# Optimization experiments

Hardware: AMD Instinct MI355X
Metric: run time of the kernel (lower is better)

The kernel has to match this reference:

```python
import jax, jax.numpy as jnp
import numpy as np

N = 10000      # nodes
E = 320000     # edges
F_IN = 33      # input node features
H = 32         # hidden
G = 64         # graphs in batch


def setup_inputs() -> dict:
    key = jax.random.key(0)
    ks = jax.random.split(key, 24)
    s = 0.1  # small init scale for numerical sanity
    inp = {
        "x": jax.random.normal(ks[0], (N, F_IN), jnp.float32),
        "edge_index": jax.random.randint(ks[1], (2, E), 0, N, jnp.int32),
        "edge_attr": jax.random.uniform(ks[2], (E, 1), jnp.float32),
        "batch": jnp.sort(jax.random.randint(ks[3], (N,), 0, G, jnp.int32)),
        # conv1: edge-MLP Linear(1 -> F_IN*H), root weight [F_IN,H], bias [H]
        "nn_w1": jax.random.normal(ks[4], (1, F_IN * H), jnp.float32) * s,
        "nn_b1": jax.random.normal(ks[5], (F_IN * H,), jnp.float32) * s,
        "root1": jax.random.normal(ks[6], (F_IN, H), jnp.float32) * s,
        "bias1": jnp.zeros((H,), jnp.float32),
        # conv2: edge-MLP Linear(1 -> H*H)
        "nn_w2": jax.random.normal(ks[7], (1, H * H), jnp.float32) * s,
        "nn_b2": jax.random.normal(ks[8], (H * H,), jnp.float32) * s,
        "root2": jax.random.normal(ks[9], (H, H), jnp.float32) * s,
        "bias2": jnp.zeros((H,), jnp.float32),
        # conv3
        "nn_w3": jax.random.normal(ks[10], (1, H * H), jnp.float32) * s,
        "nn_b3": jax.random.normal(ks[11], (H * H,), jnp.float32) * s,
        "root3": jax.random.normal(ks[12], (H, H), jnp.float32) * s,
        "bias3": jnp.zeros((H,), jnp.float32),
        # readout MLP: Linear(3H -> H), Linear(H -> 2)
        "lin1_w": jax.random.normal(ks[13], (3 * H, H), jnp.float32) * s,
        "lin1_b": jnp.zeros((H,), jnp.float32),
        "lin2_w": jax.random.normal(ks[14], (H, 2), jnp.float32) * s,
        "lin2_b": jnp.zeros((2,), jnp.float32),
    }
    return inp


def _nnconv(x, src, dst, edge_attr, nn_w, nn_b, root, bias):
    """PyG NNConv (aggr='add'): out_i = x_i @ root + bias + sum_{e: dst(e)=i} x_{src(e)} @ Theta(e_attr)."""
    in_dim, out_dim = root.shape
    # per-edge weight matrix from edge MLP: [E, in, out]
    W = (edge_attr @ nn_w + nn_b).reshape(-1, in_dim, out_dim)
    msg = jnp.einsum('ei,eio->eo', x[src], W)          # gather + per-edge small matmul
    agg = jax.ops.segment_sum(msg, dst, num_segments=N)  # scatter-add into targets
    return agg + x @ root + bias


def reference(x, edge_index, edge_attr, batch,
              nn_w1, nn_b1, root1, bias1,
              nn_w2, nn_b2, root2, bias2,
              nn_w3, nn_b3, root3, bias3,
              lin1_w, lin1_b, lin2_w, lin2_b):
    src, dst = edge_index[0], edge_index[1]
    h = jax.nn.relu(_nnconv(x, src, dst, edge_attr, nn_w1, nn_b1, root1, bias1))
    h = jax.nn.relu(_nnconv(h, src, dst, edge_attr, nn_w2, nn_b2, root2, bias2))
    h = jax.nn.relu(_nnconv(h, src, dst, edge_attr, nn_w3, nn_b3, root3, bias3))
    # global add / mean / max pooling over graphs
    add_p = jax.ops.segment_sum(h, batch, num_segments=G)
    cnt = jax.ops.segment_sum(jnp.ones((N, 1), h.dtype), batch, num_segments=G)
    mean_p = add_p / jnp.maximum(cnt, 1.0)
    max_p = jax.ops.segment_max(h, batch, num_segments=G)
    max_p = jnp.where(jnp.isfinite(max_p), max_p, 0.0)  # guard empty segments
    g = jnp.concatenate([add_p, mean_p, max_p], axis=1)  # [G, 3H]
    g = jax.nn.relu(g @ lin1_w + lin1_b)
    # dropout p=0.5 is identity in eval mode
    logits = g @ lin2_w + lin2_b
    return jax.nn.log_softmax(logits, axis=-1)
```

## Files before the change

### kernel.cpp

```cpp
#include <hip/hip_runtime.h>

constexpr int N_  = 10000;
constexpr int E_  = 320000;
constexpr int F1  = 33;
constexpr int H   = 32;
constexpr int G   = 64;
constexpr int CAP = 96;
constexpr int NB_ = 1280;
constexpr int ROW = CAP * 8;

constexpr int EBLK = E_ / 256;
constexpr int PBLK = N_ / 8;
constexpr int SLICES = 32;
constexpr int CHUNKS = 16;
constexpr int TILE   = 640;
constexpr int AT    = 1024;
constexpr int ITERS = TILE / 128;

__device__ __forceinline__ unsigned bf16r(float x) {
    unsigned u = __float_as_uint(x);
    return (u + 0x7FFFu + ((u >> 16) & 1u)) >> 16;
}

__device__ __forceinline__ size_t mslot(int n, int pos) {
    return (size_t)(n >> 3) * ROW + (size_t)(pos >> 3) * 64 + (n & 7) * 8 + (pos & 7);
}


__global__ __launch_bounds__(256) void k_build_pre1(
        const int* __restrict__ ei, const float* __restrict__ ea,
        const float* __restrict__ x, const int* __restrict__ batch,
        const float* __restrict__ A, const float* __restrict__ Bm,
        const float* __restrict__ Rw, const float* __restrict__ bias,
        int* __restrict__ counts, unsigned* __restrict__ meta2,
        unsigned* __restrict__ UVs, float* __restrict__ Rs,
        int* __restrict__ startsP) {
    __shared__ unsigned s_uv[32][9];
    __shared__ float    s_r[32][9];
    if (blockIdx.x < EBLK) {
        int e = blockIdx.x * 256 + threadIdx.x;
        int s = ei[e];
        int d = ei[E_ + e];
        int pos = atomicAdd(&counts[d], 1);
        meta2[mslot(d, pos)] = (unsigned)s | (bf16r(ea[e]) << 16);
    } else {
        int base8 = (blockIdx.x - EBLK) * 8;
        int grp = threadIdx.x >> 5;
        int f = threadIdx.x & 31;
        int node = base8 + grp;
        if (f == 0) {
            int b = batch[node];
            int bp = (node == 0) ? -1 : batch[node - 1];
            if (b != bp) startsP[b] = node + 1;
        }
        float u = 0.f, v = 0.f, r = bias[f];
        const float* xr = x + (size_t)node * F1;
        #pragma unroll
        for (int k = 0; k < F1; ++k) {
            float xv = xr[k];
            u = fmaf(xv, A[k * H + f], u);
            v = fmaf(xv, Bm[k * H + f], v);
            r = fmaf(xv, Rw[k * H + f], r);
        }
        s_uv[f][grp] = bf16r(u) | (bf16r(v) << 16);
        s_r[f][grp]  = r;
        __syncthreads();
        int fo = threadIdx.x >> 3;
        int nl = threadIdx.x & 7;
        UVs[(size_t)fo * N_ + base8 + nl] = s_uv[fo][nl];
        Rs [(size_t)fo * N_ + base8 + nl] = s_r [fo][nl];
    }
}


__global__ __launch_bounds__(256) void k_pre(
        const float* __restrict__ Hs,
        const float* __restrict__ A, const float* __restrict__ Bm,
        const float* __restrict__ Rw, const float* __restrict__ bias,
        unsigned* __restrict__ UVs, float* __restrict__ Rs) {
    __shared__ unsigned s_uv[32][9];
    __shared__ float    s_r[32][9];
    int base8 = blockIdx.x * 8;
    int grp = threadIdx.x >> 5;
    int f = threadIdx.x & 31;
    int node = base8 + grp;
    float hv = Hs[(size_t)f * N_ + node];
    float u = 0.f, v = 0.f, r = bias[f];
    #pragma unroll
    for (int k = 0; k < H; ++k) {
        float hk = __shfl(hv, k, 32);
        u = fmaf(hk, A[k * H + f], u);
        v = fmaf(hk, Bm[k * H + f], v);
        r = fmaf(hk, Rw[k * H + f], r);
    }
    s_uv[f][grp] = bf16r(u) | (bf16r(v) << 16);
    s_r[f][grp]  = r;
    __syncthreads();
    int fo = threadIdx.x >> 3;
    int nl = threadIdx.x & 7;
    UVs[(size_t)fo * N_ + base8 + nl] = s_uv[fo][nl];
    Rs [(size_t)fo * N_ + base8 + nl] = s_r [fo][nl];
}


__global__ __launch_bounds__(1024, 8) void k_agg_lds(
        const int* __restrict__ counts, const unsigned* __restrict__ meta2,
        const unsigned* __restrict__ UVs, const float* __restrict__ Rs,
        float* __restrict__ Hs) {
    __shared__ __align__(16) unsigned uvl[N_];
    int s     = blockIdx.x & 31;
    int chunk = blockIdx.x >> 5;

    int l   = threadIdx.x & 63;
    int wav = threadIdx.x >> 6;
    int j0  = l & 7;
    int nl  = l >> 3;

    int cbase = chunk * TILE + wav * 8;
    int node = cbase + nl;
    int nc = min(node, N_ - 1);
    int dg = (node < N_) ? counts[nc] : 0;
    float rv = Rs[(size_t)s * N_ + nc];
    const unsigned* mrow = meta2 + (size_t)(cbase >> 3) * ROW + l;
    unsigned m0 = mrow[0], m1 = mrow[64], m2 = mrow[128],
             m3 = mrow[192], m4 = mrow[256], m5 = mrow[320];

    const unsigned* srcp = UVs + (size_t)s * N_;
    #pragma unroll
    for (int i = 0; i < 3; ++i) {
        int d4 = (i * AT + (int)threadIdx.x) * 4;
        if (d4 + 4 <= N_) {
            uint4 t = *reinterpret_cast<const uint4*>(srcp + d4);
            *reinterpret_cast<uint4*>(&uvl[d4]) = t;
        }
    }
    __syncthreads();

    for (int it = 0; it < ITERS; ++it) {
        int nbase = cbase + 128;
        int nnode = nbase + nl;
        int nnc = min(nnode, N_ - 1);
        int ndg = 0; float nrv = 0.f;
        unsigned n0 = 0, n1 = 0, n2 = 0, n3 = 0, n4 = 0, n5 = 0;
        if (it < ITERS - 1) {
            ndg = (nnode < N_) ? counts[nnc] : 0;
            nrv = Rs[(size_t)s * N_ + nnc];
            const unsigned* nmr = meta2 + (size_t)(nbase >> 3) * ROW + l;
            n0 = nmr[0]; n1 = nmr[64]; n2 = nmr[128];
            n3 = nmr[192]; n4 = nmr[256]; n5 = nmr[320];
        }

        float acc = 0.f;
        auto slot = [&](int p, unsigned mv) {
            unsigned idx = min(mv & 0xFFFFu, (unsigned)(N_ - 1));
            unsigned w = uvl[idx];
            float t = fmaf(__uint_as_float(mv & 0xFFFF0000u),
                           __uint_as_float(w << 16),
                           __uint_as_float(w & 0xFFFF0000u));
            if (j0 + 8 * p < dg) acc += t;
        };
        slot(0, m0); slot(1, m1); slot(2, m2);
        slot(3, m3); slot(4, m4); slot(5, m5);
        if (__any(dg > 48)) {
            const unsigned* trow = meta2 + (size_t)(cbase >> 3) * ROW + l;
            for (int p = 6; __any(j0 + 8 * p < dg); ++p)
                slot(p, trow[p * 64]);
        }
        acc += __shfl_xor(acc, 1);
        acc += __shfl_xor(acc, 2);
        acc += __shfl_xor(acc, 4);
        float h = fmaxf(rv + acc, 0.f);
        if (j0 == 0 && node < N_) Hs[(size_t)s * N_ + node] = h;

        cbase = nbase; node = nnode; nc = nnc; dg = ndg; rv = nrv;
        m0 = n0; m1 = n1; m2 = n2; m3 = n3; m4 = n4; m5 = n5;
    }
}


__global__ __launch_bounds__(256) void k_pool(
        const float* __restrict__ Hs, const int* __restrict__ startsP,
        const float* __restrict__ w1, const float* __restrict__ b1,
        const float* __restrict__ w2, const float* __restrict__ b2,
        float* __restrict__ out) {
    __shared__ int sst[G];
    __shared__ float ga[32], gm[32], gx[32];
    int tid = threadIdx.x;
    if (tid < G) sst[tid] = startsP[tid];
    __syncthreads();
    int g = blockIdx.x;
    int sp = sst[g];
    int s = 0, e = 0;
    if (sp != 0) {
        s = sp - 1;
        e = N_;
        for (int j = g + 1; j < G; ++j)
            if (sst[j]) { e = sst[j] - 1; break; }
    }
    int f = tid >> 3, oct = tid & 7;
    float sum = 0.f, mx = 0.f;
    for (int n = s + oct; n < e; n += 8) {
        float w = Hs[(size_t)f * N_ + n];
        sum += w;
        mx = fmaxf(mx, w);
    }
    sum += __shfl_xor(sum, 1); mx = fmaxf(mx, __shfl_xor(mx, 1));
    sum += __shfl_xor(sum, 2); mx = fmaxf(mx, __shfl_xor(mx, 2));
    sum += __shfl_xor(sum, 4); mx = fmaxf(mx, __shfl_xor(mx, 4));
    if (oct == 0) {
        float c = fmaxf((float)(e - s), 1.0f);
        ga[f] = sum;
        gm[f] = sum / c;
        gx[f] = mx;
    }
    __syncthreads();
    if (tid < 32) {
        float hacc = b1[tid];
        #pragma unroll
        for (int k = 0; k < H; ++k) {
            hacc = fmaf(ga[k], w1[k * H + tid], hacc);
            hacc = fmaf(gm[k], w1[(H + k) * H + tid], hacc);
            hacc = fmaf(gx[k], w1[(2 * H + k) * H + tid], hacc);
        }
        float hid = fmaxf(hacc, 0.f);
        float p0 = hid * w2[tid * 2 + 0];
        float p1 = hid * w2[tid * 2 + 1];
        #pragma unroll
        for (int offq = 16; offq; offq >>= 1) {
            p0 += __shfl_xor(p0, offq, 32);
            p1 += __shfl_xor(p1, offq, 32);
        }
        if (tid == 0) {
            float l0 = p0 + b2[0], l1 = p1 + b2[1];
            float m = fmaxf(l0, l1);
            float lse = m + logf(expf(l0 - m) + expf(l1 - m));
            out[g * 2 + 0] = l0 - lse;
            out[g * 2 + 1] = l1 - lse;
        }
    }
}


extern "C" void kernel_launch(void* const* d_in, const int* in_sizes, int n_in,
                              void* d_out, int out_size, void* d_ws, size_t ws_size,
                              hipStream_t stream) {
    const float* x      = (const float*)d_in[0];
    const int*   ei     = (const int*)  d_in[1];
    const float* ea     = (const float*)d_in[2];
    const int*   batch  = (const int*)  d_in[3];
    const float* nn_w1  = (const float*)d_in[4];
    const float* nn_b1  = (const float*)d_in[5];
    const float* root1  = (const float*)d_in[6];
    const float* bias1  = (const float*)d_in[7];
    const float* nn_w2  = (const float*)d_in[8];
    const float* nn_b2  = (const float*)d_in[9];
    const float* root2  = (const float*)d_in[10];
    const float* bias2  = (const float*)d_in[11];
    const float* nn_w3  = (const float*)d_in[12];
    const float* nn_b3  = (const float*)d_in[13];
    const float* root3  = (const float*)d_in[14];
    const float* bias3  = (const float*)d_in[15];
    const float* lin1_w = (const float*)d_in[16];
    const float* lin1_b = (const float*)d_in[17];
    const float* lin2_w = (const float*)d_in[18];
    const float* lin2_b = (const float*)d_in[19];
    float* out = (float*)d_out;

    char* ws = (char*)d_ws;
    size_t off = 0;
    auto alloc = [&](size_t bytes) -> void* {
        void* p = ws + off;
        off += (bytes + 255) & ~(size_t)255;
        return p;
    };
    const size_t zbytes = N_ * sizeof(int) + G * sizeof(int);
    char* zchunk = (char*)alloc(zbytes);
    int*  counts  = (int*)zchunk;
    int*  startsP = (int*)(zchunk + N_ * sizeof(int));
    unsigned* meta2 = (unsigned*)alloc((size_t)NB_ * ROW * sizeof(unsigned));
    unsigned* UVs1 = (unsigned*)alloc((size_t)H * N_ * sizeof(unsigned));
    unsigned* UVs2 = (unsigned*)alloc((size_t)H * N_ * sizeof(unsigned));
    unsigned* UVs3 = (unsigned*)alloc((size_t)H * N_ * sizeof(unsigned));
    float* Rs1 = (float*)alloc((size_t)H * N_ * sizeof(float));
    float* Rs2 = (float*)alloc((size_t)H * N_ * sizeof(float));
    float* Rs3 = (float*)alloc((size_t)H * N_ * sizeof(float));
    float* h1  = (float*)alloc((size_t)H * N_ * sizeof(float));
    float* h2  = (float*)alloc((size_t)H * N_ * sizeof(float));
    float* h3  = (float*)alloc((size_t)H * N_ * sizeof(float));

    hipMemsetAsync(zchunk, 0, zbytes, stream);

    k_build_pre1<<<EBLK + PBLK, 256, 0, stream>>>(ei, ea, x, batch,
                                                  nn_w1, nn_b1, root1, bias1,
                                                  counts, meta2, UVs1, Rs1, startsP);

    k_agg_lds<<<SLICES * CHUNKS, AT, 0, stream>>>(counts, meta2, UVs1, Rs1, h1);
    k_pre    <<<PBLK, 256, 0, stream>>>(h1, nn_w2, nn_b2, root2, bias2, UVs2, Rs2);
    k_agg_lds<<<SLICES * CHUNKS, AT, 0, stream>>>(counts, meta2, UVs2, Rs2, h2);
    k_pre    <<<PBLK, 256, 0, stream>>>(h2, nn_w3, nn_b3, root3, bias3, UVs3, Rs3);
    k_agg_lds<<<SLICES * CHUNKS, AT, 0, stream>>>(counts, meta2, UVs3, Rs3, h3);

    k_pool<<<G, 256, 0, stream>>>(h3, startsP, lin1_w, lin1_b, lin2_w, lin2_b, out);
}
```

Before: 168.3 us.

## Process two feature slices per aggregation block with interleaved LDS table

Each aggregation block now handles two output feature slices, staging both slices' bf16 UV tables interleaved in shared memory (80KB). One 64-bit LDS read then serves both features, and each edge's metadata load and degree check is shared across the two slices. Chunks shrink to 320 nodes and the grid doubles in chunks, so the same total block count is kept. The larger LDS footprint lowers how many blocks fit per CU, and the doubled staging per block adds global reads.

New measurement: 170.3 us. About the same (+1.2%).

```diff
diff --git a/kernel.cpp b/kernel.cpp
--- a/kernel.cpp
+++ b/kernel.cpp
@@ -12,10 +12,11 @@
 constexpr int EBLK = E_ / 256;
 constexpr int PBLK = N_ / 8;
 constexpr int SLICES = 32;
-constexpr int CHUNKS = 16;
-constexpr int TILE   = 640;
-constexpr int AT    = 1024;
-constexpr int ITERS = TILE / 128;
+constexpr int PAIRS  = 16;
+constexpr int CHUNKS = 32;
+constexpr int TILE   = 320;
+constexpr int AT     = 1024;
+constexpr int ITERS  = 3;
 
 __device__ __forceinline__ unsigned bf16r(float x) {
     unsigned u = __float_as_uint(x);
@@ -107,9 +108,10 @@
         const int* __restrict__ counts, const unsigned* __restrict__ meta2,
         const unsigned* __restrict__ UVs, const float* __restrict__ Rs,
         float* __restrict__ Hs) {
-    __shared__ __align__(16) unsigned uvl[N_];
-    int s     = blockIdx.x & 31;
-    int chunk = blockIdx.x >> 5;
+    __shared__ __align__(16) unsigned uvl[2 * N_];
+    int s0    = (blockIdx.x & (PAIRS - 1)) * 2;
+    int s1    = s0 + 1;
+    int chunk = blockIdx.x >> 4;
 
     int l   = threadIdx.x & 63;
     int wav = threadIdx.x >> 6;
@@ -120,18 +122,22 @@
     int node = cbase + nl;
     int nc = min(node, N_ - 1);
     int dg = (node < N_) ? counts[nc] : 0;
-    float rv = Rs[(size_t)s * N_ + nc];
-    const unsigned* mrow = meta2 + (size_t)(cbase >> 3) * ROW + l;
+    float rv0 = Rs[(size_t)s0 * N_ + nc];
+    float rv1 = Rs[(size_t)s1 * N_ + nc];
+    const unsigned* mrow = meta2 + (size_t)min(cbase >> 3, NB_ - 1) * ROW + l;
     unsigned m0 = mrow[0], m1 = mrow[64], m2 = mrow[128],
              m3 = mrow[192], m4 = mrow[256], m5 = mrow[320];
 
-    const unsigned* srcp = UVs + (size_t)s * N_;
+    const unsigned* p0 = UVs + (size_t)s0 * N_;
+    const unsigned* p1 = UVs + (size_t)s1 * N_;
     #pragma unroll
     for (int i = 0; i < 3; ++i) {
-        int d4 = (i * AT + (int)threadIdx.x) * 4;
-        if (d4 + 4 <= N_) {
-            uint4 t = *reinterpret_cast<const uint4*>(srcp + d4);
-            *reinterpret_cast<uint4*>(&uvl[d4]) = t;
+        int q = i * AT + (int)threadIdx.x;
+        if (q * 4 + 4 <= N_) {
+            uint4 a = *reinterpret_cast<const uint4*>(p0 + q * 4);
+            uint4 b = *reinterpret_cast<const uint4*>(p1 + q * 4);
+            *reinterpret_cast<uint4*>(&uvl[q * 8])     = make_uint4(a.x, b.x, a.y, b.y);
+            *reinterpret_cast<uint4*>(&uvl[q * 8 + 4]) = make_uint4(a.z, b.z, a.w, b.w);
         }
     }
     __syncthreads();
@@ -140,39 +146,44 @@
         int nbase = cbase + 128;
         int nnode = nbase + nl;
         int nnc = min(nnode, N_ - 1);
-        int ndg = 0; float nrv = 0.f;
+        int ndg = 0; float nrv0 = 0.f, nrv1 = 0.f;
         unsigned n0 = 0, n1 = 0, n2 = 0, n3 = 0, n4 = 0, n5 = 0;
         if (it < ITERS - 1) {
             ndg = (nnode < N_) ? counts[nnc] : 0;
-            nrv = Rs[(size_t)s * N_ + nnc];
-            const unsigned* nmr = meta2 + (size_t)(nbase >> 3) * ROW + l;
+            nrv0 = Rs[(size_t)s0 * N_ + nnc];
+            nrv1 = Rs[(size_t)s1 * N_ + nnc];
+            const unsigned* nmr = meta2 + (size_t)min(nbase >> 3, NB_ - 1) * ROW + l;
             n0 = nmr[0]; n1 = nmr[64]; n2 = nmr[128];
             n3 = nmr[192]; n4 = nmr[256]; n5 = nmr[320];
         }
 
-        float acc = 0.f;
+        float acc0 = 0.f, acc1 = 0.f;
         auto slot = [&](int p, unsigned mv) {
             unsigned idx = min(mv & 0xFFFFu, (unsigned)(N_ - 1));
-            unsigned w = uvl[idx];
-            float t = fmaf(__uint_as_float(mv & 0xFFFF0000u),
-                           __uint_as_float(w << 16),
-                           __uint_as_float(w & 0xFFFF0000u));
-            if (j0 + 8 * p < dg) acc += t;
+            uint2 w = *reinterpret_cast<const uint2*>(uvl + 2 * idx);
+            float a = __uint_as_float(mv & 0xFFFF0000u);
+            float t0 = fmaf(a, __uint_as_float(w.x << 16),
+                            __uint_as_float(w.x & 0xFFFF0000u));
+            float t1 = fmaf(a, __uint_as_float(w.y << 16),
+                            __uint_as_float(w.y & 0xFFFF0000u));
+            if (j0 + 8 * p < dg) { acc0 += t0; acc1 += t1; }
         };
         slot(0, m0); slot(1, m1); slot(2, m2);
         slot(3, m3); slot(4, m4); slot(5, m5);
         if (__any(dg > 48)) {
-            const unsigned* trow = meta2 + (size_t)(cbase >> 3) * ROW + l;
+            const unsigned* trow = meta2 + (size_t)min(cbase >> 3, NB_ - 1) * ROW + l;
             for (int p = 6; __any(j0 + 8 * p < dg); ++p)
                 slot(p, trow[p * 64]);
         }
-        acc += __shfl_xor(acc, 1);
-        acc += __shfl_xor(acc, 2);
-        acc += __shfl_xor(acc, 4);
-        float h = fmaxf(rv + acc, 0.f);
-        if (j0 == 0 && node < N_) Hs[(size_t)s * N_ + node] = h;
-
-        cbase = nbase; node = nnode; nc = nnc; dg = ndg; rv = nrv;
+        acc0 += __shfl_xor(acc0, 1); acc1 += __shfl_xor(acc1, 1);
+        acc0 += __shfl_xor(acc0, 2); acc1 += __shfl_xor(acc1, 2);
+        acc0 += __shfl_xor(acc0, 4); acc1 += __shfl_xor(acc1, 4);
+        if (j0 == 0 && node < N_) {
+            Hs[(size_t)s0 * N_ + node] = fmaxf(rv0 + acc0, 0.f);
+            Hs[(size_t)s1 * N_ + node] = fmaxf(rv1 + acc1, 0.f);
+        }
+
+        cbase = nbase; node = nnode; nc = nnc; dg = ndg; rv0 = nrv0; rv1 = nrv1;
         m0 = n0; m1 = n1; m2 = n2; m3 = n3; m4 = n4; m5 = n5;
     }
 }
@@ -294,11 +305,11 @@
                                                   nn_w1, nn_b1, root1, bias1,
                                                   counts, meta2, UVs1, Rs1, startsP);
 
-    k_agg_lds<<<SLICES * CHUNKS, AT, 0, stream>>>(counts, meta2, UVs1, Rs1, h1);
+    k_agg_lds<<<PAIRS * CHUNKS, AT, 0, stream>>>(counts, meta2, UVs1, Rs1, h1);
     k_pre    <<<PBLK, 256, 0, stream>>>(h1, nn_w2, nn_b2, root2, bias2, UVs2, Rs2);
-    k_agg_lds<<<SLICES * CHUNKS, AT, 0, stream>>>(counts, meta2, UVs2, Rs2, h2);
+    k_agg_lds<<<PAIRS * CHUNKS, AT, 0, stream>>>(counts, meta2, UVs2, Rs2, h2);
     k_pre    <<<PBLK, 256, 0, stream>>>(h2, nn_w3, nn_b3, root3, bias3, UVs3, Rs3);
-    k_agg_lds<<<SLICES * CHUNKS, AT, 0, stream>>>(counts, meta2, UVs3, Rs3, h3);
+    k_agg_lds<<<PAIRS * CHUNKS, AT, 0, stream>>>(counts, meta2, UVs3, Rs3, h3);
 
     k_pool<<<G, 256, 0, stream>>>(h3, startsP, lin1_w, lin1_b, lin2_w, lin2_b, out);
 }
```
